# Optimization experiments

Hardware: AMD Instinct MI355X
Metric: run time of the kernel (lower is better)

Reference implementation:

```python
import jax, jax.numpy as jnp
import numpy as np

KH, KW = 7, 7
PAD = ((KH // 2, KH // 2), (KW // 2, KW // 2))


def _box_conv(x, w):
    # x: [B, 1, H, W], w: [1, 1, KH, KW]
    return jax.lax.conv_general_dilated(
        x, w,
        window_strides=(1, 1),
        padding=PAD,
        dimension_numbers=('NCHW', 'OIHW', 'NCHW'),
    )


def setup_inputs() -> dict:
    key = jax.random.key(0)
    k_img, = jax.random.split(key, 1)
    image = jax.random.normal(k_img, (16, 1, 1024, 1024), dtype=jnp.float32)
    # Conv weight initialized to uniform box filter 1/(KH*KW), as in PatchStd.__init__
    weight = jnp.full((1, 1, KH, KW), 1.0 / (KH * KW), dtype=jnp.float32)
    return {"image": image, "weight": weight}


def reference(image, weight):
    # var = E[x^2] - E[x]^2 within local window, then sqrt
    mean_sq = _box_conv(image * image, weight)
    mean = _box_conv(image, weight)
    return jnp.sqrt(mean_sq - mean * mean)
```

## Files before the change

kernel.cpp:

```cpp
#include <hip/hip_runtime.h>


#define IMG_W 1024
#define IMG_H 1024
#define SH    16
#define TPB   256
#define NR    (SH + 6)
#define RING  4
#define SEGF  320

typedef float v4f __attribute__((ext_vector_type(4)));

#define WAITV(N) asm volatile("s_waitcnt vmcnt(" #N ")" ::: "memory")

__global__ __launch_bounds__(TPB) void patchstd_kernel(
    const float* __restrict__ img, const float* __restrict__ wptr,
    float* __restrict__ out)
{
    __shared__ float lds[4 * RING * SEGF];

    const int tx   = threadIdx.x;
    const int w_   = tx >> 6;
    const int lane = tx & 63;
    const int c0   = tx << 2;
    const int y0   = blockIdx.y * SH;
    const float* base  = img + (size_t)blockIdx.z * (IMG_W * IMG_H);
    float*       obase = out + (size_t)blockIdx.z * (IMG_W * IMG_H);
    const float w = wptr[0];

    const int Sw   = 256 * w_ - 8;
    const int colA = min(max(Sw + 4 * lane, 0), IMG_W - 4);
    const int colB = min(max(Sw + 256 + lane, 0), IMG_W - 1);
    const float* gA = base + colA;
    const float* gB = base + colB;
    float* const seg0 = &lds[w_ * (RING * SEGF)];

    auto issue = [&](int j) {
        const int rc = min(max(y0 - 3 + j, 0), IMG_H - 1);
        const size_t ro = (size_t)rc * IMG_W;
        float* sl = seg0 + (j & (RING - 1)) * SEGF;
        __builtin_amdgcn_global_load_lds(
            (const __attribute__((address_space(1))) void*)(gA + ro),
            (__attribute__((address_space(3))) void*)sl, 16, 0, 0);
        __builtin_amdgcn_global_load_lds(
            (const __attribute__((address_space(1))) void*)(gB + ro),
            (__attribute__((address_space(3))) void*)(sl + 256), 4, 0, 0);
    };

    auto hsum = [&](const float* v, float* h, float* q) {
        float s = v[1]+v[2]+v[3]+v[4]+v[5]+v[6]+v[7];
        h[0] = s;
        s = s - v[1] + v[8];  h[1] = s;
        s = s - v[2] + v[9];  h[2] = s;
        h[3] = s - v[3] + v[10];
        float sq[11];
        #pragma unroll
        for (int i = 1; i <= 10; ++i) sq[i] = v[i] * v[i];
        float t = sq[1]+sq[2]+sq[3]+sq[4]+sq[5]+sq[6]+sq[7];
        q[0] = t;
        t = t - sq[1] + sq[8];  q[1] = t;
        t = t - sq[2] + sq[9];  q[2] = t;
        q[3] = t - sq[3] + sq[10];
    };

    float rh[7][4], rq[7][4];
    float vh[4] = {0.f,0.f,0.f,0.f};
    float vq[4] = {0.f,0.f,0.f,0.f};

    issue(0); issue(1); issue(2);

    #pragma unroll
    for (int j = 0; j < NR; ++j) {
        if (j + 3 < NR) issue(j + 3);

        if      (j <= 6)  WAITV(6);
        else if (j == 7)  WAITV(7);
        else if (j == 8)  WAITV(8);
        else if (j <= 18) WAITV(9);
        else if (j == 19) WAITV(7);
        else if (j == 20) WAITV(5);
        else              WAITV(3);

        const float* seg = seg0 + (j & (RING - 1)) * SEGF;
        const v4f* p = (const v4f*)(seg + 4 * lane + 4);
        v4f A = p[0], B = p[1], C = p[2];
        float v[12] = {A.x,A.y,A.z,A.w, B.x,B.y,B.z,B.w, C.x,C.y,C.z,C.w};
        if (tx == 0)   { v[0]=0.f; v[1]=0.f; v[2]=0.f;  v[3]=0.f;  }
        if (tx == 255) { v[8]=0.f; v[9]=0.f; v[10]=0.f; v[11]=0.f; }

        float h[4], q[4];
        const int R = y0 - 3 + j;
        if (R < 0 || R >= IMG_H) {
            #pragma unroll
            for (int k = 0; k < 4; ++k) { h[k] = 0.f; q[k] = 0.f; }
        } else {
            hsum(v, h, q);
        }

        if (j < 6) {
            #pragma unroll
            for (int k = 0; k < 4; ++k) {
                rh[j][k] = h[k]; rq[j][k] = q[k];
                vh[k] += h[k];   vq[k] += q[k];
            }
            if (j == 5) {
                #pragma unroll
                for (int k = 0; k < 4; ++k) { rh[6][k] = 0.f; rq[6][k] = 0.f; }
            }
        } else {
            const int s = j % 7;
            float o[4];
            #pragma unroll
            for (int k = 0; k < 4; ++k) {
                vh[k] += h[k] - rh[s][k];
                vq[k] += q[k] - rq[s][k];
                rh[s][k] = h[k]; rq[s][k] = q[k];
                float mean = w * vh[k];
                float var  = fmaf(w, vq[k], -(mean * mean));
                o[k] = __builtin_amdgcn_sqrtf(fmaxf(var, 0.f));
            }
            *reinterpret_cast<float4*>(obase + (size_t)(y0 + j - 6) * IMG_W + c0) =
                make_float4(o[0], o[1], o[2], o[3]);
        }
    }
}

extern "C" void kernel_launch(void* const* d_in, const int* in_sizes, int n_in,
                              void* d_out, int out_size, void* d_ws, size_t ws_size,
                              hipStream_t stream) {
    const float* img = (const float*)d_in[0];
    const float* wt  = (const float*)d_in[1];
    float* out = (float*)d_out;
    const int batch = in_sizes[0] / (IMG_W * IMG_H);
    dim3 grid(1, IMG_H / SH, batch);
    patchstd_kernel<<<grid, dim3(TPB, 1, 1), 0, stream>>>(img, wt, out);
}
```

Baseline: 29.00 us.

## Split image width across two blocks with two output columns per thread

The grid now splits each row into 512-column halves, so each thread produces two output columns instead of four and the block count doubles. Each wave loads one 16-byte-per-lane LDS segment covering 128 columns plus halo, which removes the second narrow halo load and shrinks the LDS ring. The vmcnt waits are retuned for one load per row. In exchange, the halo traffic per output column goes up, and odd lanes now select an unaligned window out of a 12-float LDS read.

New measurement: 32.34 us. 1.12x slower.

```diff
diff --git a/kernel.cpp b/kernel.cpp
--- a/kernel.cpp
+++ b/kernel.cpp
@@ -7,9 +7,10 @@
 #define TPB   256
 #define NR    (SH + 6)
 #define RING  4
-#define SEGF  320
+#define SEGF  256
 
 typedef float v4f __attribute__((ext_vector_type(4)));
+typedef float v2f __attribute__((ext_vector_type(2)));
 
 #define WAITV(N) asm volatile("s_waitcnt vmcnt(" #N ")" ::: "memory")
 
@@ -22,50 +23,33 @@
     const int tx   = threadIdx.x;
     const int w_   = tx >> 6;
     const int lane = tx & 63;
-    const int c0   = tx << 2;
     const int y0   = blockIdx.y * SH;
     const float* base  = img + (size_t)blockIdx.z * (IMG_W * IMG_H);
     float*       obase = out + (size_t)blockIdx.z * (IMG_W * IMG_H);
     const float w = wptr[0];
 
-    const int Sw   = 256 * w_ - 8;
-    const int colA = min(max(Sw + 4 * lane, 0), IMG_W - 4);
-    const int colB = min(max(Sw + 256 + lane, 0), IMG_W - 1);
+    const int W0    = 512 * blockIdx.x + 128 * w_;
+    const int SO    = W0 - 8;
+    const int gcol0 = W0 + 2 * lane;
+    const int colA = min(max(SO + 4 * lane, 0), IMG_W - 4);
     const float* gA = base + colA;
-    const float* gB = base + colB;
     float* const seg0 = &lds[w_ * (RING * SEGF)];
 
     auto issue = [&](int j) {
         const int rc = min(max(y0 - 3 + j, 0), IMG_H - 1);
-        const size_t ro = (size_t)rc * IMG_W;
         float* sl = seg0 + (j & (RING - 1)) * SEGF;
         __builtin_amdgcn_global_load_lds(
-            (const __attribute__((address_space(1))) void*)(gA + ro),
+            (const __attribute__((address_space(1))) void*)(gA + (size_t)rc * IMG_W),
             (__attribute__((address_space(3))) void*)sl, 16, 0, 0);
-        __builtin_amdgcn_global_load_lds(
-            (const __attribute__((address_space(1))) void*)(gB + ro),
-            (__attribute__((address_space(3))) void*)(sl + 256), 4, 0, 0);
     };
 
-    auto hsum = [&](const float* v, float* h, float* q) {
-        float s = v[1]+v[2]+v[3]+v[4]+v[5]+v[6]+v[7];
-        h[0] = s;
-        s = s - v[1] + v[8];  h[1] = s;
-        s = s - v[2] + v[9];  h[2] = s;
-        h[3] = s - v[3] + v[10];
-        float sq[11];
-        #pragma unroll
-        for (int i = 1; i <= 10; ++i) sq[i] = v[i] * v[i];
-        float t = sq[1]+sq[2]+sq[3]+sq[4]+sq[5]+sq[6]+sq[7];
-        q[0] = t;
-        t = t - sq[1] + sq[8];  q[1] = t;
-        t = t - sq[2] + sq[9];  q[2] = t;
-        q[3] = t - sq[3] + sq[10];
-    };
+    float rh[7][2], rq[7][2];
+    float vh[2] = {0.f, 0.f};
+    float vq[2] = {0.f, 0.f};
 
-    float rh[7][4], rq[7][4];
-    float vh[4] = {0.f,0.f,0.f,0.f};
-    float vq[4] = {0.f,0.f,0.f,0.f};
+    const int f0 = (2 * lane + 5) & ~3;
+    const bool odd = (lane & 1);
+    const float* segq0 = seg0 + f0;
 
     issue(0); issue(1); issue(2);
 
@@ -73,45 +57,55 @@
     for (int j = 0; j < NR; ++j) {
         if (j + 3 < NR) issue(j + 3);
 
-        if      (j <= 6)  WAITV(6);
-        else if (j == 7)  WAITV(7);
-        else if (j == 8)  WAITV(8);
-        else if (j <= 18) WAITV(9);
-        else if (j == 19) WAITV(7);
-        else if (j == 20) WAITV(5);
+        if      (j <= 6)  WAITV(3);
+        else if (j == 7)  WAITV(4);
+        else if (j == 8)  WAITV(5);
+        else if (j <= 18) WAITV(6);
+        else if (j == 19) WAITV(5);
+        else if (j == 20) WAITV(4);
         else              WAITV(3);
 
-        const float* seg = seg0 + (j & (RING - 1)) * SEGF;
-        const v4f* p = (const v4f*)(seg + 4 * lane + 4);
+        const v4f* p = (const v4f*)(segq0 + (j & (RING - 1)) * SEGF);
         v4f A = p[0], B = p[1], C = p[2];
-        float v[12] = {A.x,A.y,A.z,A.w, B.x,B.y,B.z,B.w, C.x,C.y,C.z,C.w};
-        if (tx == 0)   { v[0]=0.f; v[1]=0.f; v[2]=0.f;  v[3]=0.f;  }
-        if (tx == 255) { v[8]=0.f; v[9]=0.f; v[10]=0.f; v[11]=0.f; }
+        float raw[12] = {A.x,A.y,A.z,A.w, B.x,B.y,B.z,B.w, C.x,C.y,C.z,C.w};
+        float v[8];
+        #pragma unroll
+        for (int i = 0; i < 8; ++i) v[i] = odd ? raw[3 + i] : raw[1 + i];
+        if (gcol0 == 0)    { v[0]=0.f; v[1]=0.f; v[2]=0.f; }
+        if (gcol0 == 2)    { v[0]=0.f; }
+        if (gcol0 == 1020) { v[7]=0.f; }
+        if (gcol0 == 1022) { v[5]=0.f; v[6]=0.f; v[7]=0.f; }
 
-        float h[4], q[4];
+        float h[2], q[2];
         const int R = y0 - 3 + j;
         if (R < 0 || R >= IMG_H) {
+            h[0]=0.f; h[1]=0.f; q[0]=0.f; q[1]=0.f;
+        } else {
+            float s = v[0]+v[1]+v[2]+v[3]+v[4]+v[5]+v[6];
+            h[0] = s;
+            h[1] = s - v[0] + v[7];
+            float sq[8];
             #pragma unroll
-            for (int k = 0; k < 4; ++k) { h[k] = 0.f; q[k] = 0.f; }
-        } else {
-            hsum(v, h, q);
+            for (int i = 0; i < 8; ++i) sq[i] = v[i] * v[i];
+            float t = sq[0]+sq[1]+sq[2]+sq[3]+sq[4]+sq[5]+sq[6];
+            q[0] = t;
+            q[1] = t - sq[0] + sq[7];
         }
 
         if (j < 6) {
             #pragma unroll
-            for (int k = 0; k < 4; ++k) {
+            for (int k = 0; k < 2; ++k) {
                 rh[j][k] = h[k]; rq[j][k] = q[k];
                 vh[k] += h[k];   vq[k] += q[k];
             }
             if (j == 5) {
-                #pragma unroll
-                for (int k = 0; k < 4; ++k) { rh[6][k] = 0.f; rq[6][k] = 0.f; }
+                rh[6][0]=0.f; rh[6][1]=0.f; rq[6][0]=0.f; rq[6][1]=0.f;
             }
         } else {
             const int s = j % 7;
-            float o[4];
+            float o[2];
             #pragma unroll
-            for (int k = 0; k < 4; ++k) {
+            for (int k = 0; k < 2; ++k) {
                 vh[k] += h[k] - rh[s][k];
                 vq[k] += q[k] - rq[s][k];
                 rh[s][k] = h[k]; rq[s][k] = q[k];
@@ -119,8 +113,8 @@
                 float var  = fmaf(w, vq[k], -(mean * mean));
                 o[k] = __builtin_amdgcn_sqrtf(fmaxf(var, 0.f));
             }
-            *reinterpret_cast<float4*>(obase + (size_t)(y0 + j - 6) * IMG_W + c0) =
-                make_float4(o[0], o[1], o[2], o[3]);
+            v2f ov; ov.x = o[0]; ov.y = o[1];
+            *reinterpret_cast<v2f*>(obase + (size_t)(y0 + j - 6) * IMG_W + gcol0) = ov;
         }
     }
 }
@@ -132,6 +126,6 @@
     const float* wt  = (const float*)d_in[1];
     float* out = (float*)d_out;
     const int batch = in_sizes[0] / (IMG_W * IMG_H);
-    dim3 grid(1, IMG_H / SH, batch);
+    dim3 grid(IMG_W / 512, IMG_H / SH, batch);
     patchstd_kernel<<<grid, dim3(TPB, 1, 1), 0, stream>>>(img, wt, out);
 }
```
